# Kernel tuning notes

Measured on AMD Instinct MI355X. Metric: run time of the kernel, lower is better.

Reference implementation:

```python
import jax, jax.numpy as jnp
import numpy as np

D_MODEL = 1024
N_HEADS = 16
HEAD_DIM = D_MODEL // N_HEADS
D_FF = 4096
EPS = 1e-5
THETA = 10000.0
B, S = 2, 2048


def _rope_cache(seq_len, head_dim, theta=THETA):
    inv_freq = 1.0 / theta ** (jnp.arange(0, head_dim, 2, dtype=jnp.float32) / head_dim)
    t = jnp.arange(seq_len, dtype=jnp.float32)
    freqs = jnp.einsum('i,j->ij', t, inv_freq)          # [S, head_dim//2]
    emb = jnp.concatenate([freqs, freqs], axis=-1)       # [S, head_dim]
    return jnp.cos(emb), jnp.sin(emb)


def _rotate_half(x):
    x1, x2 = jnp.split(x, 2, axis=-1)
    return jnp.concatenate([-x2, x1], axis=-1)


def _ada_rmsnorm(x, time_emb, weight, w1, b1, w2, b2):
    # time_mlp: Linear -> SiLU -> Linear producing [B, 2*D]
    h = jax.nn.silu(time_emb @ w1 + b1)
    scale, shift = jnp.split(h @ w2 + b2, 2, axis=-1)    # each [B, D]
    norm = x * jax.lax.rsqrt(jnp.mean(x * x, axis=-1, keepdims=True) + EPS)
    return norm * weight * (1.0 + scale[:, None, :]) + shift[:, None, :]


def setup_inputs() -> dict:
    key = jax.random.key(0)
    ks = jax.random.split(key, 24)
    rn = lambda k, shp: (jax.random.normal(k, shp, dtype=jnp.float32) * 0.02)
    return {
        'x': jax.random.normal(ks[0], (B, S, D_MODEL), dtype=jnp.float32),
        'time_emb': jax.random.normal(ks[1], (B, D_MODEL), dtype=jnp.float32),
        # norm1
        'w_norm1': jnp.ones((D_MODEL,), jnp.float32),
        't1_w1': rn(ks[2], (D_MODEL, D_MODEL)), 't1_b1': jnp.zeros((D_MODEL,), jnp.float32),
        't1_w2': rn(ks[3], (D_MODEL, 2 * D_MODEL)), 't1_b2': jnp.zeros((2 * D_MODEL,), jnp.float32),
        # norm2
        'w_norm2': jnp.ones((D_MODEL,), jnp.float32),
        't2_w1': rn(ks[4], (D_MODEL, D_MODEL)), 't2_b1': jnp.zeros((D_MODEL,), jnp.float32),
        't2_w2': rn(ks[5], (D_MODEL, 2 * D_MODEL)), 't2_b2': jnp.zeros((2 * D_MODEL,), jnp.float32),
        # attention projections (stored [in, out])
        'wq': rn(ks[6], (D_MODEL, D_MODEL)), 'bq': jnp.zeros((D_MODEL,), jnp.float32),
        'wk': rn(ks[7], (D_MODEL, D_MODEL)), 'bk': jnp.zeros((D_MODEL,), jnp.float32),
        'wv': rn(ks[8], (D_MODEL, D_MODEL)), 'bv': jnp.zeros((D_MODEL,), jnp.float32),
        'wo': rn(ks[9], (D_MODEL, D_MODEL)), 'bo': jnp.zeros((D_MODEL,), jnp.float32),
        # GLU FFN (no bias)
        'w_gate': rn(ks[10], (D_MODEL, D_FF)),
        'w_up': rn(ks[11], (D_MODEL, D_FF)),
        'w_down': rn(ks[12], (D_FF, D_MODEL)),
    }


def reference(x, time_emb,
              w_norm1, t1_w1, t1_b1, t1_w2, t1_b2,
              w_norm2, t2_w1, t2_b1, t2_w2, t2_b2,
              wq, bq, wk, bk, wv, bv, wo, bo,
              w_gate, w_up, w_down):
    b, s, _ = x.shape
    cos, sin = _rope_cache(s, HEAD_DIM)                  # [S, head_dim]

    # --- attention sub-block ---
    nx = _ada_rmsnorm(x, time_emb, w_norm1, t1_w1, t1_b1, t1_w2, t1_b2)
    q = (nx @ wq + bq).reshape(b, s, N_HEADS, HEAD_DIM)
    k = (nx @ wk + bk).reshape(b, s, N_HEADS, HEAD_DIM)
    v = (nx @ wv + bv).reshape(b, s, N_HEADS, HEAD_DIM)
    c = cos[:, None, :]  # [S,1,head_dim] broadcasts over heads
    si = sin[:, None, :]
    q = q * c + _rotate_half(q) * si
    k = k * c + _rotate_half(k) * si
    scores = jnp.einsum('bshd,bthd->bhst', q, k) / jnp.sqrt(jnp.float32(HEAD_DIM))
    probs = jax.nn.softmax(scores, axis=-1)
    attn = jnp.einsum('bhst,bthd->bshd', probs, v).reshape(b, s, D_MODEL)
    x = x + attn @ wo + bo

    # --- GLU FFN sub-block ---
    nx = _ada_rmsnorm(x, time_emb, w_norm2, t2_w1, t2_b1, t2_w2, t2_b2)
    gate = jax.nn.gelu(nx @ w_gate, approximate=False)
    ff = (gate * (nx @ w_up)) @ w_down
    return x + ff
```

## Files before the change

kernel.cpp:

```cpp
#include <hip/hip_runtime.h>
#include <hip/hip_bf16.h>

typedef __bf16 bf16_t;
typedef __bf16 bf16x8 __attribute__((ext_vector_type(8)));
typedef float f32x4 __attribute__((ext_vector_type(4)));

typedef __attribute__((address_space(3))) void lds_void_t;
typedef const __attribute__((address_space(1))) void gbl_void_t;

static constexpr int S_LEN = 2048;
static constexpr int NBATCH = 2;
static constexpr int DM = 1024;
static constexpr int NH = 16;
static constexpr int HD = 64;
static constexpr int DFF = 4096;
static constexpr int MROWS = NBATCH * S_LEN;
static constexpr int QKVN = 3072;

__global__ __launch_bounds__(256) void rope_table_k(float* __restrict__ cs) {
  int idx = blockIdx.x * 256 + threadIdx.x;
  int i = idx & 31, s = idx >> 5;
  float inv = powf(10000.0f, -(float)i / 32.0f);
  float ang = (float)s * inv;
  float c = cosf(ang), sn = sinf(ang);
  cs[s * 64 + i] = c;  cs[s * 64 + i + 32] = c;
  cs[S_LEN * 64 + s * 64 + i] = sn;  cs[S_LEN * 64 + s * 64 + i + 32] = sn;
}

__global__ __launch_bounds__(256) void gemv_k(const float* __restrict__ vin,
    const float* __restrict__ W, const float* __restrict__ bias,
    float* __restrict__ out, int N, int dosilu) {
  int b = blockIdx.y;
  int tj = threadIdx.x & 31, ti = threadIdx.x >> 5;
  int j = blockIdx.x * 32 + tj;
  const float* v = vin + b * DM;
  float acc = 0.f;
  int i0 = ti * 128;
#pragma unroll 8
  for (int i = i0; i < i0 + 128; ++i) acc += v[i] * W[(size_t)i * N + j];
  __shared__ float red[8][32];
  red[ti][tj] = acc;
  __syncthreads();
  if (threadIdx.x < 32) {
    float a = 0.f;
#pragma unroll
    for (int t = 0; t < 8; ++t) a += red[t][threadIdx.x];
    a += bias[j - tj + threadIdx.x];
    if (dosilu) a = a / (1.0f + expf(-a));
    out[(size_t)b * N + blockIdx.x * 32 + threadIdx.x] = a;
  }
}

__global__ __launch_bounds__(256) void bcat_k(const float* __restrict__ bq,
    const float* __restrict__ bk, const float* __restrict__ bv, float* __restrict__ o) {
  int i = blockIdx.x * 256 + threadIdx.x;
  o[i] = i < 1024 ? bq[i] : (i < 2048 ? bk[i - 1024] : bv[i - 2048]);
}

template<typename T>
__global__ __launch_bounds__(256) void ada_rms_k(const T* __restrict__ x,
    const float* __restrict__ wnorm, const float* __restrict__ ss,
    bf16_t* __restrict__ out) {
  int row = blockIdx.x;
  int b = row >> 11;
  const T* xr = x + (size_t)row * DM;
  float xl[4]; float s = 0.f;
#pragma unroll
  for (int i = 0; i < 4; ++i) { xl[i] = (float)xr[threadIdx.x + i * 256]; s += xl[i] * xl[i]; }
#pragma unroll
  for (int d = 1; d < 64; d <<= 1) s += __shfl_xor(s, d);
  __shared__ float red[4];
  int w = threadIdx.x >> 6;
  if ((threadIdx.x & 63) == 0) red[w] = s;
  __syncthreads();
  s = red[0] + red[1] + red[2] + red[3];
  float r = rsqrtf(s * (1.0f / DM) + 1e-5f);
  bf16_t* orow = out + (size_t)row * DM;
#pragma unroll
  for (int i = 0; i < 4; ++i) {
    int j = threadIdx.x + i * 256;
    float sc = ss[b * 2048 + j], sh = ss[b * 2048 + 1024 + j];
    orow[j] = (bf16_t)(xl[i] * r * wnorm[j] * (1.0f + sc) + sh);
  }
}

__global__ __launch_bounds__(256) void conv_t_k(const float* __restrict__ in,
    bf16_t* __restrict__ out, int K, int N, int ilv) {
  __shared__ float t[32][33];
  int n0 = blockIdx.x * 32, k0 = blockIdx.y * 32;
  int tx = threadIdx.x & 31, ty = threadIdx.x >> 5;
#pragma unroll
  for (int i = 0; i < 32; i += 8)
    t[ty + i][tx] = in[(size_t)(k0 + ty + i) * N + n0 + tx];
  __syncthreads();
#pragma unroll
  for (int i = 0; i < 32; i += 8) {
    int n = n0 + ty + i;
    int row = (ilv == 0) ? n : ((n >> 4) * 32 + (n & 15) + (ilv == 2 ? 16 : 0));
    out[(size_t)row * K + k0 + tx] = (bf16_t)t[tx][ty + i];
  }
}

template<int EPI>
__global__ __launch_bounds__(256) void gemm_bt(
    const bf16_t* __restrict__ A, const bf16_t* __restrict__ BT,
    int M, int N, int K,
    const float* __restrict__ bias, const float* __restrict__ residf,
    const bf16_t* __restrict__ residb, bf16_t* outb, float* outf,
    const float* __restrict__ cstab, bf16_t* __restrict__ vt) {
  const int col0 = blockIdx.x * 128, row0 = blockIdx.y * 128;
  const int tid = threadIdx.x, l = tid & 63, w = tid >> 6;
  const int wr = (w >> 1) * 64, wc = (w & 1) * 64;
  const int lo = l & 15, hi = l >> 4;
  __shared__ __align__(16) bf16_t lA[2][128][64];
  __shared__ __align__(16) bf16_t lB[2][128][64];
  f32x4 zero = {0.f, 0.f, 0.f, 0.f};
  f32x4 acc[4][4];
#pragma unroll
  for (int m = 0; m < 4; ++m)
#pragma unroll
    for (int n = 0; n < 4; ++n) acc[m][n] = zero;

  const int lrow = l >> 3;
  const int swzb = ((l & 7) ^ lrow) * 16;

  auto stage = [&](int buf, int k0) {
#pragma unroll
    for (int i = 0; i < 4; ++i) {
      int rbase = w * 32 + i * 8;
      const char* gA = (const char*)&A[(size_t)(row0 + rbase + lrow) * K + k0] + swzb;
      const char* gB = (const char*)&BT[(size_t)(col0 + rbase + lrow) * K + k0] + swzb;
      __builtin_amdgcn_global_load_lds((gbl_void_t*)gA, (lds_void_t*)&lA[buf][rbase][0], 16, 0, 0);
      __builtin_amdgcn_global_load_lds((gbl_void_t*)gB, (lds_void_t*)&lB[buf][rbase][0], 16, 0, 0);
    }
  };

  const int NT = K >> 6;
  stage(0, 0);
  __syncthreads();
  int cur = 0;
  for (int t = 0; t < NT; ++t) {
    if (t + 1 < NT) stage(cur ^ 1, (t + 1) << 6);
#pragma unroll
    for (int kk = 0; kk < 64; kk += 32) {
      bf16x8 af[4], bfr[4];
#pragma unroll
      for (int m = 0; m < 4; ++m)
        af[m] = *(const bf16x8*)&lA[cur][wr + m * 16 + lo][((((kk >> 3) + hi)) ^ (lo & 7)) * 8];
#pragma unroll
      for (int n = 0; n < 4; ++n)
        bfr[n] = *(const bf16x8*)&lB[cur][wc + n * 16 + lo][((((kk >> 3) + hi)) ^ (lo & 7)) * 8];
#pragma unroll
      for (int m = 0; m < 4; ++m)
#pragma unroll
        for (int n = 0; n < 4; ++n)
          acc[m][n] = __builtin_amdgcn_mfma_f32_16x16x32_bf16(af[m], bfr[n], acc[m][n], 0, 0, 0);
    }
    __syncthreads();
    cur ^= 1;
  }

  if (EPI == 5) {
    if (col0 >= 2048) {
#pragma unroll
      for (int m = 0; m < 4; ++m) {
#pragma unroll
        for (int n = 0; n < 4; ++n) {
          int cl = col0 + wc + n * 16 + lo;
          int r0 = row0 + wr + m * 16 + hi * 4;
          int dfull = cl - 2048;
          int bh = (r0 >> 11) * 16 + (dfull >> 6);
          int d = dfull & 63;
          float bb = bias[cl];
          __align__(8) bf16_t tmp[4];
#pragma unroll
          for (int j = 0; j < 4; ++j) tmp[j] = (bf16_t)(acc[m][n][j] + bb);
          *(uint2*)&vt[((size_t)bh * 64 + d) * S_LEN + (r0 & 2047)] = *(uint2*)tmp;
        }
      }
    } else {
#pragma unroll
      for (int m = 0; m < 4; ++m) {
#pragma unroll
        for (int n = 0; n < 2; ++n) {
          int cl = col0 + wc + n * 16 + lo;
          int i = cl & 63;
          float b1 = bias[cl], b2 = bias[cl + 32];
          float scale = (cl < 1024) ? 0.125f : 1.0f;
#pragma unroll
          for (int j = 0; j < 4; ++j) {
            int r = row0 + wr + m * 16 + hi * 4 + j;
            int s = r & 2047;
            float c = cstab[s * 64 + i], sn = cstab[S_LEN * 64 + s * 64 + i];
            float x1 = acc[m][n][j] + b1, x2 = acc[m][n + 2][j] + b2;
            size_t idx = (size_t)r * N + cl;
            outb[idx]      = (bf16_t)((x1 * c - x2 * sn) * scale);
            outb[idx + 32] = (bf16_t)((x2 * c + x1 * sn) * scale);
          }
        }
      }
    }
    return;
  }

  if (EPI == 6) {
#pragma unroll
    for (int m = 0; m < 4; ++m) {
#pragma unroll
      for (int p = 0; p < 2; ++p) {
        int clg = col0 + wc + 2 * p * 16;
        int jcol = ((clg >> 5) << 4) + lo;
#pragma unroll
        for (int j = 0; j < 4; ++j) {
          int r = row0 + wr + m * 16 + hi * 4 + j;
          float g = acc[m][2 * p][j];
          float u = acc[m][2 * p + 1][j];
          g = 0.5f * g * (1.0f + erff(g * 0.70710678118f));
          outb[(size_t)r * DFF + jcol] = (bf16_t)(g * u);
        }
      }
    }
    return;
  }

#pragma unroll
  for (int m = 0; m < 4; ++m) {
#pragma unroll
    for (int n = 0; n < 4; ++n) {
#pragma unroll
      for (int j = 0; j < 4; ++j) {
        int r = row0 + wr + m * 16 + hi * 4 + j;
        int cl = col0 + wc + n * 16 + lo;
        size_t idx = (size_t)r * N + cl;
        float vv = acc[m][n][j];
        if (EPI == 1)      { vv += bias[cl] + residf[idx]; outb[idx] = (bf16_t)vv; }
        else               { vv += (float)residb[idx]; outf[idx] = vv; }
      }
    }
  }
}

__global__ __launch_bounds__(512, 4) void attn_k(const bf16_t* __restrict__ qk,
    const bf16_t* __restrict__ vt, bf16_t* __restrict__ o) {
  int g = blockIdx.x;
  int orig = (g & 7) * 64 + (g >> 3);
  int qblk = orig & 15;
  int bh = orig >> 4;
  int b = bh >> 4, h = bh & 15;
  const int q0 = qblk * 128;
  const int tid = threadIdx.x, l = tid & 63, w = tid >> 6;
  const int lo = l & 15, hi = l >> 4;

  __shared__ __align__(16) bf16_t lk[128][72];
  __shared__ __align__(16) bf16_t lvt[64][136];
  __shared__ __align__(16) bf16_t lp[8][16][136];

  bf16x8 qf[2];
#pragma unroll
  for (int ks = 0; ks < 2; ++ks)
    qf[ks] = *(const bf16x8*)&qk[((size_t)(b * S_LEN) + q0 + w * 16 + lo) * QKVN
                                 + h * HD + ks * 32 + hi * 8];

  f32x4 zero = {0.f, 0.f, 0.f, 0.f};
  f32x4 oa[4];
#pragma unroll
  for (int n = 0; n < 4; ++n) oa[n] = zero;
  float mrow[4], lrow[4];
#pragma unroll
  for (int j = 0; j < 4; ++j) { mrow[j] = -1e30f; lrow[j] = 0.f; }

  const size_t kbase = (size_t)(b * S_LEN) * QKVN + 1024 + h * HD;
  const size_t vbase = (size_t)bh * 64 * S_LEN;

  for (int t0 = 0; t0 < S_LEN; t0 += 128) {
    __syncthreads();
#pragma unroll
    for (int it = 0; it < 2; ++it) {
      int idx = it * 512 + tid;
      int r = idx >> 3, dc = (idx & 7) * 8;
      *(uint4*)&lk[r][dc] = *(const uint4*)&qk[kbase + (size_t)(t0 + r) * QKVN + dc];
      int d = idx >> 4, sc = (idx & 15) * 8;
      *(uint4*)&lvt[d][sc] = *(const uint4*)&vt[vbase + (size_t)d * S_LEN + t0 + sc];
    }
    __syncthreads();

    f32x4 s[8];
#pragma unroll
    for (int n = 0; n < 8; ++n) s[n] = zero;
    __builtin_amdgcn_s_setprio(1);
#pragma unroll
    for (int ks = 0; ks < 2; ++ks) {
#pragma unroll
      for (int n = 0; n < 8; ++n) {
        bf16x8 bk = *(const bf16x8*)&lk[n * 16 + lo][ks * 32 + hi * 8];
        s[n] = __builtin_amdgcn_mfma_f32_16x16x32_bf16(qf[ks], bk, s[n], 0, 0, 0);
      }
    }
    __builtin_amdgcn_s_setprio(0);

#pragma unroll
    for (int j = 0; j < 4; ++j) {
      float mx = fmaxf(fmaxf(fmaxf(s[0][j], s[1][j]), fmaxf(s[2][j], s[3][j])),
                       fmaxf(fmaxf(s[4][j], s[5][j]), fmaxf(s[6][j], s[7][j])));
      mx = fmaxf(mx, __shfl_xor(mx, 1));
      mx = fmaxf(mx, __shfl_xor(mx, 2));
      mx = fmaxf(mx, __shfl_xor(mx, 4));
      mx = fmaxf(mx, __shfl_xor(mx, 8));
      if (__any(mx > mrow[j] + 8.0f)) {
        float mn = fmaxf(mrow[j], mx);
        float corr = __expf(mrow[j] - mn);
        mrow[j] = mn;
        lrow[j] *= corr;
#pragma unroll
        for (int n = 0; n < 4; ++n) oa[n][j] *= corr;
      }
      float psum = 0.f;
#pragma unroll
      for (int n = 0; n < 8; ++n) {
        float p = __expf(s[n][j] - mrow[j]);
        psum += p;
        lp[w][hi * 4 + j][n * 16 + lo] = (bf16_t)p;
      }
      lrow[j] += psum;
    }

    __builtin_amdgcn_s_setprio(1);
#pragma unroll
    for (int kk = 0; kk < 128; kk += 32) {
      bf16x8 ap = *(const bf16x8*)&lp[w][lo][kk + hi * 8];
#pragma unroll
      for (int n = 0; n < 4; ++n) {
        bf16x8 bv = *(const bf16x8*)&lvt[n * 16 + lo][kk + hi * 8];
        oa[n] = __builtin_amdgcn_mfma_f32_16x16x32_bf16(ap, bv, oa[n], 0, 0, 0);
      }
    }
    __builtin_amdgcn_s_setprio(0);
  }

#pragma unroll
  for (int j = 0; j < 4; ++j) {
    float ls = lrow[j];
    ls += __shfl_xor(ls, 1); ls += __shfl_xor(ls, 2);
    ls += __shfl_xor(ls, 4); ls += __shfl_xor(ls, 8);
    float inv = 1.0f / ls;
    int row = q0 + w * 16 + hi * 4 + j;
#pragma unroll
    for (int n = 0; n < 4; ++n)
      o[((size_t)(b * S_LEN) + row) * DM + h * HD + n * 16 + lo] = (bf16_t)(oa[n][j] * inv);
  }
}

extern "C" void kernel_launch(void* const* d_in, const int* in_sizes, int n_in,
                              void* d_out, int out_size, void* d_ws, size_t ws_size,
                              hipStream_t stream) {
  const float* x    = (const float*)d_in[0];
  const float* te   = (const float*)d_in[1];
  const float* wn1  = (const float*)d_in[2];
  const float* t1w1 = (const float*)d_in[3];
  const float* t1b1 = (const float*)d_in[4];
  const float* t1w2 = (const float*)d_in[5];
  const float* t1b2 = (const float*)d_in[6];
  const float* wn2  = (const float*)d_in[7];
  const float* t2w1 = (const float*)d_in[8];
  const float* t2b1 = (const float*)d_in[9];
  const float* t2w2 = (const float*)d_in[10];
  const float* t2b2 = (const float*)d_in[11];
  const float* wq   = (const float*)d_in[12];
  const float* bq   = (const float*)d_in[13];
  const float* wk   = (const float*)d_in[14];
  const float* bk   = (const float*)d_in[15];
  const float* wv   = (const float*)d_in[16];
  const float* bv   = (const float*)d_in[17];
  const float* wo   = (const float*)d_in[18];
  const float* bo   = (const float*)d_in[19];
  const float* wg   = (const float*)d_in[20];
  const float* wu   = (const float*)d_in[21];
  const float* wd   = (const float*)d_in[22];
  float* out = (float*)d_out;

  char* ws = (char*)d_ws;
  const size_t MB = 1ull << 20;
  bf16_t* woT   = (bf16_t*)(ws + 0 * MB);
  bf16_t* wguT  = (bf16_t*)(ws + 2 * MB);
  bf16_t* wdT   = (bf16_t*)(ws + 18 * MB);
  bf16_t* nx    = (bf16_t*)(ws + 26 * MB);
  bf16_t* wqkvT = (bf16_t*)(ws + 34 * MB);
  bf16_t* qkvb  = (bf16_t*)(ws + 40 * MB);
  bf16_t* vt    = (bf16_t*)(ws + 64 * MB);
  bf16_t* gb    = (bf16_t*)(ws + 40 * MB);
  bf16_t* attnb = (bf16_t*)(ws + 72 * MB);
  bf16_t* x2b   = (bf16_t*)(ws + 80 * MB);
  float*  cs    = (float*)(ws + 88 * MB);
  float*  ss1   = (float*)(ws + 89 * MB);
  float*  ss2   = (float*)(ws + 89 * MB + 16384);
  float*  htmp  = (float*)(ws + 89 * MB + 32768);
  float*  bcat  = (float*)(ws + 89 * MB + 40960);

  rope_table_k<<<256, 256, 0, stream>>>(cs);
  bcat_k<<<12, 256, 0, stream>>>(bq, bk, bv, bcat);
  gemv_k<<<dim3(32, 2), 256, 0, stream>>>(te, t1w1, t1b1, htmp, 1024, 1);
  gemv_k<<<dim3(64, 2), 256, 0, stream>>>(htmp, t1w2, t1b2, ss1, 2048, 0);
  gemv_k<<<dim3(32, 2), 256, 0, stream>>>(te, t2w1, t2b1, htmp, 1024, 1);
  gemv_k<<<dim3(64, 2), 256, 0, stream>>>(htmp, t2w2, t2b2, ss2, 2048, 0);

  conv_t_k<<<dim3(32, 32),  256, 0, stream>>>(wq, wqkvT,               1024, 1024, 0);
  conv_t_k<<<dim3(32, 32),  256, 0, stream>>>(wk, wqkvT + 1024 * 1024, 1024, 1024, 0);
  conv_t_k<<<dim3(32, 32),  256, 0, stream>>>(wv, wqkvT + 2048 * 1024, 1024, 1024, 0);
  conv_t_k<<<dim3(32, 32),  256, 0, stream>>>(wo, woT, 1024, 1024, 0);
  conv_t_k<<<dim3(128, 32), 256, 0, stream>>>(wg, wguT, 1024, 4096, 1);
  conv_t_k<<<dim3(128, 32), 256, 0, stream>>>(wu, wguT, 1024, 4096, 2);
  conv_t_k<<<dim3(32, 128), 256, 0, stream>>>(wd, wdT, 4096, 1024, 0);

  ada_rms_k<float><<<MROWS, 256, 0, stream>>>(x, wn1, ss1, nx);

  gemm_bt<5><<<dim3(24, 32), 256, 0, stream>>>(nx, wqkvT, MROWS, QKVN, DM,
                                               bcat, nullptr, nullptr, qkvb, nullptr, cs, vt);

  attn_k<<<512, 512, 0, stream>>>(qkvb, vt, attnb);

  gemm_bt<1><<<dim3(8, 32), 256, 0, stream>>>(attnb, woT, MROWS, DM, DM,
                                              bo, x, nullptr, x2b, nullptr, nullptr, nullptr);

  ada_rms_k<bf16_t><<<MROWS, 256, 0, stream>>>(x2b, wn2, ss2, nx);

  gemm_bt<6><<<dim3(64, 32), 256, 0, stream>>>(nx, wguT, MROWS, 2 * DFF, DM,
                                               nullptr, nullptr, nullptr, gb, nullptr, nullptr, nullptr);
  gemm_bt<4><<<dim3(8, 32), 256, 0, stream>>>(gb, wdT, MROWS, DM, DFF,
                                              nullptr, nullptr, x2b, nullptr, out, nullptr, nullptr);
}
```

Before: 373.2 us.

## Prefetch attention K/V tiles into registers and use BK=128 for narrow GEMMs

The attention kernel now loads the next K and V^T tile from global memory into registers while it computes on the current LDS tile, then writes them to LDS after the PV step, overlapping global latency with MFMA work. The GEMM template gains a BK parameter with a 16-way XOR swizzle for 128-wide K tiles, used for the two N=1024 GEMMs (output projection and down projection), which launch only 256 blocks. This halves the number of K-loop iterations and barriers for those GEMMs, at the cost of doubled LDS per block (64KB) and extra registers in attention, which may reduce occupancy.

```diff
diff --git a/kernel.cpp b/kernel.cpp
--- a/kernel.cpp
+++ b/kernel.cpp
@@ -101,7 +101,7 @@
   }
 }
 
-template<int EPI>
+template<int EPI, int BK>
 __global__ __launch_bounds__(256) void gemm_bt(
     const bf16_t* __restrict__ A, const bf16_t* __restrict__ BT,
     int M, int N, int K,
@@ -112,8 +112,8 @@
   const int tid = threadIdx.x, l = tid & 63, w = tid >> 6;
   const int wr = (w >> 1) * 64, wc = (w & 1) * 64;
   const int lo = l & 15, hi = l >> 4;
-  __shared__ __align__(16) bf16_t lA[2][128][64];
-  __shared__ __align__(16) bf16_t lB[2][128][64];
+  __shared__ __align__(16) bf16_t lA[2][128][BK];
+  __shared__ __align__(16) bf16_t lB[2][128][BK];
   f32x4 zero = {0.f, 0.f, 0.f, 0.f};
   f32x4 acc[4][4];
 #pragma unroll
@@ -121,35 +121,49 @@
 #pragma unroll
     for (int n = 0; n < 4; ++n) acc[m][n] = zero;
 
-  const int lrow = l >> 3;
-  const int swzb = ((l & 7) ^ lrow) * 16;
-
   auto stage = [&](int buf, int k0) {
-#pragma unroll
-    for (int i = 0; i < 4; ++i) {
-      int rbase = w * 32 + i * 8;
-      const char* gA = (const char*)&A[(size_t)(row0 + rbase + lrow) * K + k0] + swzb;
-      const char* gB = (const char*)&BT[(size_t)(col0 + rbase + lrow) * K + k0] + swzb;
-      __builtin_amdgcn_global_load_lds((gbl_void_t*)gA, (lds_void_t*)&lA[buf][rbase][0], 16, 0, 0);
-      __builtin_amdgcn_global_load_lds((gbl_void_t*)gB, (lds_void_t*)&lB[buf][rbase][0], 16, 0, 0);
+    if constexpr (BK == 64) {
+      const int lrow = l >> 3;
+      const int swzb = ((l & 7) ^ lrow) * 16;
+#pragma unroll
+      for (int i = 0; i < 4; ++i) {
+        int rbase = w * 32 + i * 8;
+        const char* gA = (const char*)&A[(size_t)(row0 + rbase + lrow) * K + k0] + swzb;
+        const char* gB = (const char*)&BT[(size_t)(col0 + rbase + lrow) * K + k0] + swzb;
+        __builtin_amdgcn_global_load_lds((gbl_void_t*)gA, (lds_void_t*)&lA[buf][rbase][0], 16, 0, 0);
+        __builtin_amdgcn_global_load_lds((gbl_void_t*)gB, (lds_void_t*)&lB[buf][rbase][0], 16, 0, 0);
+      }
+    } else {
+      const int lrow = l >> 4;
+#pragma unroll
+      for (int i = 0; i < 8; ++i) {
+        int rbase = w * 32 + i * 4;
+        int key = (i * 4 + lrow) & 15;
+        int swzb = ((l & 15) ^ key) * 16;
+        const char* gA = (const char*)&A[(size_t)(row0 + rbase + lrow) * K + k0] + swzb;
+        const char* gB = (const char*)&BT[(size_t)(col0 + rbase + lrow) * K + k0] + swzb;
+        __builtin_amdgcn_global_load_lds((gbl_void_t*)gA, (lds_void_t*)&lA[buf][rbase][0], 16, 0, 0);
+        __builtin_amdgcn_global_load_lds((gbl_void_t*)gB, (lds_void_t*)&lB[buf][rbase][0], 16, 0, 0);
+      }
     }
   };
 
-  const int NT = K >> 6;
+  const int cmask = (BK == 64) ? (lo & 7) : lo;
+  const int NT = K / BK;
   stage(0, 0);
   __syncthreads();
   int cur = 0;
   for (int t = 0; t < NT; ++t) {
-    if (t + 1 < NT) stage(cur ^ 1, (t + 1) << 6);
-#pragma unroll
-    for (int kk = 0; kk < 64; kk += 32) {
+    if (t + 1 < NT) stage(cur ^ 1, (t + 1) * BK);
+#pragma unroll
+    for (int kk = 0; kk < BK; kk += 32) {
       bf16x8 af[4], bfr[4];
 #pragma unroll
       for (int m = 0; m < 4; ++m)
-        af[m] = *(const bf16x8*)&lA[cur][wr + m * 16 + lo][((((kk >> 3) + hi)) ^ (lo & 7)) * 8];
+        af[m] = *(const bf16x8*)&lA[cur][wr + m * 16 + lo][(((kk >> 3) + hi) ^ cmask) * 8];
 #pragma unroll
       for (int n = 0; n < 4; ++n)
-        bfr[n] = *(const bf16x8*)&lB[cur][wc + n * 16 + lo][((((kk >> 3) + hi)) ^ (lo & 7)) * 8];
+        bfr[n] = *(const bf16x8*)&lB[cur][wc + n * 16 + lo][(((kk >> 3) + hi) ^ cmask) * 8];
 #pragma unroll
       for (int m = 0; m < 4; ++m)
 #pragma unroll
@@ -261,28 +275,45 @@
     qf[ks] = *(const bf16x8*)&qk[((size_t)(b * S_LEN) + q0 + w * 16 + lo) * QKVN
                                  + h * HD + ks * 32 + hi * 8];
 
-  f32x4 zero = {0.f, 0.f, 0.f, 0.f};
-  f32x4 oa[4];
-#pragma unroll
-  for (int n = 0; n < 4; ++n) oa[n] = zero;
-  float mrow[4], lrow[4];
-#pragma unroll
-  for (int j = 0; j < 4; ++j) { mrow[j] = -1e30f; lrow[j] = 0.f; }
-
   const size_t kbase = (size_t)(b * S_LEN) * QKVN + 1024 + h * HD;
   const size_t vbase = (size_t)bh * 64 * S_LEN;
 
-  for (int t0 = 0; t0 < S_LEN; t0 += 128) {
-    __syncthreads();
+  uint4 kr[2], vr[2];
+  auto ldtile = [&](int t0) {
 #pragma unroll
     for (int it = 0; it < 2; ++it) {
       int idx = it * 512 + tid;
       int r = idx >> 3, dc = (idx & 7) * 8;
-      *(uint4*)&lk[r][dc] = *(const uint4*)&qk[kbase + (size_t)(t0 + r) * QKVN + dc];
+      kr[it] = *(const uint4*)&qk[kbase + (size_t)(t0 + r) * QKVN + dc];
       int d = idx >> 4, sc = (idx & 15) * 8;
-      *(uint4*)&lvt[d][sc] = *(const uint4*)&vt[vbase + (size_t)d * S_LEN + t0 + sc];
-    }
-    __syncthreads();
+      vr[it] = *(const uint4*)&vt[vbase + (size_t)d * S_LEN + t0 + sc];
+    }
+  };
+  auto sttile = [&]() {
+#pragma unroll
+    for (int it = 0; it < 2; ++it) {
+      int idx = it * 512 + tid;
+      int r = idx >> 3, dc = (idx & 7) * 8;
+      *(uint4*)&lk[r][dc] = kr[it];
+      int d = idx >> 4, sc = (idx & 15) * 8;
+      *(uint4*)&lvt[d][sc] = vr[it];
+    }
+  };
+
+  f32x4 zero = {0.f, 0.f, 0.f, 0.f};
+  f32x4 oa[4];
+#pragma unroll
+  for (int n = 0; n < 4; ++n) oa[n] = zero;
+  float mrow[4], lrow[4];
+#pragma unroll
+  for (int j = 0; j < 4; ++j) { mrow[j] = -1e30f; lrow[j] = 0.f; }
+
+  ldtile(0);
+  sttile();
+  __syncthreads();
+
+  for (int t0 = 0; t0 < S_LEN; t0 += 128) {
+    if (t0 + 128 < S_LEN) ldtile(t0 + 128);
 
     f32x4 s[8];
 #pragma unroll
@@ -335,6 +366,12 @@
       }
     }
     __builtin_amdgcn_s_setprio(0);
+
+    if (t0 + 128 < S_LEN) {
+      __syncthreads();
+      sttile();
+      __syncthreads();
+    }
   }
 
 #pragma unroll
@@ -413,18 +450,18 @@
 
   ada_rms_k<float><<<MROWS, 256, 0, stream>>>(x, wn1, ss1, nx);
 
-  gemm_bt<5><<<dim3(24, 32), 256, 0, stream>>>(nx, wqkvT, MROWS, QKVN, DM,
-                                               bcat, nullptr, nullptr, qkvb, nullptr, cs, vt);
+  gemm_bt<5, 64><<<dim3(24, 32), 256, 0, stream>>>(nx, wqkvT, MROWS, QKVN, DM,
+                                                   bcat, nullptr, nullptr, qkvb, nullptr, cs, vt);
 
   attn_k<<<512, 512, 0, stream>>>(qkvb, vt, attnb);
 
-  gemm_bt<1><<<dim3(8, 32), 256, 0, stream>>>(attnb, woT, MROWS, DM, DM,
-                                              bo, x, nullptr, x2b, nullptr, nullptr, nullptr);
+  gemm_bt<1, 128><<<dim3(8, 32), 256, 0, stream>>>(attnb, woT, MROWS, DM, DM,
+                                                   bo, x, nullptr, x2b, nullptr, nullptr, nullptr);
 
   ada_rms_k<bf16_t><<<MROWS, 256, 0, stream>>>(x2b, wn2, ss2, nx);
 
-  gemm_bt<6><<<dim3(64, 32), 256, 0, stream>>>(nx, wguT, MROWS, 2 * DFF, DM,
-                                               nullptr, nullptr, nullptr, gb, nullptr, nullptr, nullptr);
-  gemm_bt<4><<<dim3(8, 32), 256, 0, stream>>>(gb, wdT, MROWS, DM, DFF,
-                                              nullptr, nullptr, x2b, nullptr, out, nullptr, nullptr);
-}
+  gemm_bt<6, 64><<<dim3(64, 32), 256, 0, stream>>>(nx, wguT, MROWS, 2 * DFF, DM,
+                                                   nullptr, nullptr, nullptr, gb, nullptr, nullptr, nullptr);
+  gemm_bt<4, 128><<<dim3(8, 32), 256, 0, stream>>>(gb, wdT, MROWS, DM, DFF,
+                                                   nullptr, nullptr, x2b, nullptr, out, nullptr, nullptr);
+}
```

After: 390.1 us. 1.05x slower.
